# Kernel optimization log

Measured on AMD Instinct MI355X. Metric: run time of the kernel, lower is better.

Reference implementation:

```python
import jax, jax.numpy as jnp
import numpy as np

N_QUBITS = 12
N_LAYERS = 6
BATCH = 512
DIM = 2 ** N_QUBITS


def _apply_1q(psi, G, wire):
    """Apply a single-qubit gate on `wire` (wire 0 = most significant).
    psi: [B, 2^n] complex. G: [2,2] (shared) or [B,2,2] (batched)."""
    B = psi.shape[0]
    left = 2 ** wire
    psi = psi.reshape(B, left, 2, -1)
    if G.ndim == 2:
        psi = jnp.einsum('ij,bxjy->bxiy', G, psi)
    else:
        psi = jnp.einsum('bij,bxjy->bxiy', G, psi)
    return psi.reshape(B, -1)


def _apply_cnot(psi, c, t):
    """CNOT with control c, target t on [B, 2^n] state."""
    B = psi.shape[0]
    ps = psi.reshape((B,) + (2,) * N_QUBITS)
    ca, ta = c + 1, t + 1
    c0 = jnp.take(ps, 0, axis=ca)
    c1 = jnp.take(ps, 1, axis=ca)
    flip_ax = ta if ta < ca else ta - 1
    c1 = jnp.flip(c1, axis=flip_ax)  # X on target within control=1 block
    ps = jnp.stack([c0, c1], axis=ca)
    return ps.reshape(B, -1)


def _circuit(x, weights):
    B = x.shape[0]
    psi = jnp.zeros((B, DIM), jnp.complex64).at[:, 0].set(1.0)

    # AngleEmbedding: RY(x_w) on each wire (batched gate matrices)
    h = 0.5 * x
    c, s = jnp.cos(h).astype(jnp.complex64), jnp.sin(h).astype(jnp.complex64)
    for w in range(N_QUBITS):
        G = jnp.stack([jnp.stack([c[:, w], -s[:, w]], -1),
                       jnp.stack([s[:, w], c[:, w]], -1)], -2)  # [B,2,2]
        psi = _apply_1q(psi, G, w)

    # StronglyEntanglingLayers: Rot(phi,theta,omega) per wire, then ring of CNOTs
    for l in range(N_LAYERS):
        phi, theta, omega = weights[l, :, 0], weights[l, :, 1], weights[l, :, 2]
        ct = jnp.cos(0.5 * theta).astype(jnp.complex64)
        st = jnp.sin(0.5 * theta).astype(jnp.complex64)
        ep = jnp.exp(-0.5j * (phi + omega).astype(jnp.complex64))
        em = jnp.exp(0.5j * (phi - omega).astype(jnp.complex64))
        # Rot = RZ(omega) RY(theta) RZ(phi)
        m00 = ep * ct
        m01 = -em * st
        m10 = jnp.conj(em) * st
        m11 = jnp.conj(ep) * ct
        for w in range(N_QUBITS):
            G = jnp.array([[m00[w], m01[w]], [m10[w], m11[w]]], jnp.complex64)
            psi = _apply_1q(psi, G, w)
        r = l % (N_QUBITS - 1) + 1
        for w in range(N_QUBITS):
            psi = _apply_cnot(psi, w, (w + r) % N_QUBITS)

    # <Z_w> for every wire
    probs = psi.real ** 2 + psi.imag ** 2  # [B, 2^n]
    exps = []
    for w in range(N_QUBITS):
        p = probs.reshape(B, 2 ** w, 2, -1)
        exps.append(p[:, :, 0, :].sum((1, 2)) - p[:, :, 1, :].sum((1, 2)))
    return jnp.stack(exps, -1)  # [B, n_qubits]


def setup_inputs() -> dict:
    key = jax.random.key(0)
    k1, k2, k3, k4 = jax.random.split(key, 4)
    x = jax.random.uniform(k1, (BATCH, N_QUBITS), jnp.float32, -np.pi, np.pi)
    weights = jax.random.uniform(k2, (N_LAYERS, N_QUBITS, 3), jnp.float32, 0.0, 2.0 * np.pi)
    W = jax.random.normal(k3, (1, N_QUBITS), jnp.float32) * 0.3
    b = jax.random.normal(k4, (1,), jnp.float32) * 0.01
    return {"x": x, "weights": weights, "W": W, "b": b}


def reference(x, weights, W, b):
    z = _circuit(x, weights)              # [B, n_qubits]
    y = z @ W.T + b                       # [B, 1]
    return y.squeeze(-1)                  # [B]
```

## Files before the change

kernel.cpp:

```cpp
#include <hip/hip_runtime.h>
#include <stdint.h>

#define NQ 12
#define DIM 4096
#define NLAYERS 6
#define TPB 256

typedef float v2f __attribute__((ext_vector_type(2)));

struct Pass_t {
    uint32_t WT[8];
    uint32_t WL[16];
    uint32_t RT[8];
    uint32_t RL[16];
};
struct CK_t {
    Pass_t PG2, PG3;
    Pass_t P1[NLAYERS];
    uint32_t frow[NQ];
};

constexpr uint32_t G2f(uint32_t k){ return ((k&15u)<<8) | (k&0xF0u) | ((k>>8)&15u); }
constexpr uint32_t G3f(uint32_t k){ return ((k&15u)<<4) | ((k>>4)&15u) | (k&0xF00u); }

constexpr uint32_t ech_reduce(const uint32_t* v, int n, uint32_t x){
    bool ch = true;
    while (ch) {
        ch = false;
        for (int i = 0; i < n; i++)
            if (v[i] && (x ^ v[i]) < x) { x ^= v[i]; ch = true; }
    }
    return x;
}

constexpr Pass_t build_pass(const uint32_t* Mc) {
    Pass_t P{};
    uint32_t rows[12]{}; int nr = 0;
    {
        uint32_t e1[4]{}, e2[4]{}; int n1 = 0, n2 = 0;
        for (int step = 0; step < 4; step++) {
            bool found = false;
            for (int pc = 1; pc <= 3 && !found; pc++) {
                for (int a = 0; a < 12 && !found; a++)
                for (int b = (pc >= 2 ? a + 1 : 12); (pc >= 2 ? b < 12 : b == 12) && !found; b++)
                for (int c = (pc == 3 ? b + 1 : 12); (pc == 3 ? c < 12 : c == 12) && !found; c++) {
                    uint32_t m = (1u << a);
                    if (pc >= 2) m |= (1u << b);
                    if (pc == 3) m |= (1u << c);
                    uint32_t v1 = (m >> 4) & 15u;
                    uint32_t v2 = 0;
                    for (int j = 0; j < 4; j++)
                        v2 |= (uint32_t)(__builtin_popcount(m & Mc[4 + j]) & 1) << j;
                    uint32_t r1 = ech_reduce(e1, n1, v1);
                    uint32_t r2 = ech_reduce(e2, n2, v2);
                    if (r1 && r2) {
                        rows[nr++] = m; e1[n1++] = r1; e2[n2++] = r2; found = true;
                    }
                }
            }
            if (!found) { rows[nr] = 1u << (4 + nr); nr++; }
        }
    }
    {
        uint32_t ef[12]{}; int nf = 0;
        for (int i = 0; i < nr; i++) {
            uint32_t r = ech_reduce(ef, nf, rows[i]);
            if (r) ef[nf++] = r;
        }
        for (uint32_t m = 1; m < 4096u && nr < 12; m++) {
            uint32_t r = ech_reduce(ef, nf, m);
            if (r) { rows[nr++] = m; ef[nf++] = r; }
        }
    }
    uint32_t col[12]{}, rc[12]{};
    for (int j = 0; j < 12; j++) {
        uint32_t c = 0;
        for (int i = 0; i < 12; i++) c |= (uint32_t)((rows[i] >> j) & 1u) << i;
        col[j] = c;
    }
    for (int j = 0; j < 12; j++) {
        uint32_t a = 0, mc = Mc[j];
        for (int q = 0; q < 12; q++) if ((mc >> q) & 1u) a ^= col[q];
        rc[j] = a;
    }
    for (int j = 0; j < 8; j++) { P.WT[j] = col[4 + j]; P.RT[j] = rc[4 + j]; }
    for (int l = 0; l < 16; l++) {
        uint32_t aw = 0, ar = 0;
        for (int q = 0; q < 4; q++) if ((l >> q) & 1) { aw ^= col[q]; ar ^= rc[q]; }
        P.WL[l] = aw; P.RL[l] = ar;
    }
    return P;
}

constexpr CK_t build_ck() {
    CK_t ck{};
    uint32_t Acols[NLAYERS][NQ]{}, Aicol5[NQ]{};
    for (int l = 0; l < NLAYERS; l++) {
        int r = l % (NQ - 1) + 1;
        for (int q = 0; q < NQ; q++) {
            uint32_t v = 1u << q;
            for (int w = NQ - 1; w >= 0; w--) {
                int pc = NQ - 1 - w, pt = NQ - 1 - ((w + r) % NQ);
                v ^= ((v >> pc) & 1u) << pt;
            }
            Acols[l][q] = v;
            if (l == NLAYERS - 1) {
                uint32_t u = 1u << q;
                for (int w = 0; w < NQ; w++) {
                    int pc = NQ - 1 - w, pt = NQ - 1 - ((w + r) % NQ);
                    u ^= ((u >> pc) & 1u) << pt;
                }
                Aicol5[q] = u;
            }
        }
    }
    uint32_t McG2[12]{}, McG3[12]{}, Mc1[12]{};
    for (int j = 0; j < 12; j++) { McG2[j] = G2f(1u << j); McG3[j] = G3f(1u << j); }
    ck.PG2 = build_pass(McG2);
    ck.PG3 = build_pass(McG3);
    for (int l = 1; l < NLAYERS; l++) {
        for (int j = 0; j < 12; j++) Mc1[j] = G3f(G2f(Acols[l - 1][j]));
        ck.P1[l] = build_pass(Mc1);
    }
    uint32_t Mcol[NQ]{};
    for (int j = 0; j < NQ; j++) {
        uint32_t pj = G2f(G3f(1u << j));
        uint32_t M = 0;
        for (int m = 0; m < NQ; m++) if ((pj >> m) & 1u) M ^= Aicol5[m];
        Mcol[j] = M;
    }
    for (int p = 0; p < NQ; p++) {
        uint32_t s = 0;
        for (int j = 0; j < NQ; j++) s |= ((Mcol[j] >> p) & 1u) << j;
        ck.frow[p] = s;
    }
    return ck;
}
constexpr CK_t CK = build_ck();

template<int KIND, int L, int PAR>
__device__ __forceinline__ void do_pass(v2f (&Z)[16], v2f* xb, int tid) {
    constexpr Pass_t P = (KIND == 1) ? CK.P1[L] : (KIND == 2) ? CK.PG2 : CK.PG3;
    v2f* buf = xb + PAR * DIM;
    uint32_t comb = 0;
    #pragma unroll
    for (int j = 0; j < 8; j++) {
        uint32_t pk = P.WT[j] | (P.RT[j] << 16);
        comb ^= (uint32_t)(-(int)((tid >> j) & 1)) & pk;
    }
    uint32_t wbase = comb & 0xFFFu, rbase = comb >> 16;
    #pragma unroll
    for (int l = 0; l < 16; l++)
        buf[wbase ^ P.WL[l]] = Z[l];
    __syncthreads();
    #pragma unroll
    for (int l = 0; l < 16; l++)
        Z[l] = buf[rbase ^ P.RL[l]];
}

template<int L, int W, int Q>
__device__ __forceinline__ void reg_gate(v2f (&Z)[16], const float4* smat) {
    float4 m = smat[L * NQ + W];
    #pragma unroll
    for (int l = 0; l < 16; l++) {
        if (l & (1 << Q)) continue;
        int l2 = l | (1 << Q);
        v2f z0 = Z[l], z1 = Z[l2];
        v2f j0 = { -z0.y, z0.x };
        v2f j1 = { -z1.y, z1.x };
        Z[l]  = m.x * z0 + m.y * j0 + m.z * z1 + m.w * j1;
        Z[l2] = m.x * z1 - m.y * j1 - m.z * z0 + m.w * j0;
    }
}

template<int L>
__device__ __forceinline__ void do_layer(v2f (&Z)[16], const float4* smat,
                                         v2f* xb, int tid) {
    if constexpr (L > 0)
        do_pass<1, L, (3 * L - 1) & 1>(Z, xb, tid);
    reg_gate<L, 11, 0>(Z, smat);
    reg_gate<L, 10, 1>(Z, smat);
    reg_gate<L,  9, 2>(Z, smat);
    reg_gate<L,  8, 3>(Z, smat);
    do_pass<2, L, (3 * L) & 1>(Z, xb, tid);
    reg_gate<L, 3, 0>(Z, smat);
    reg_gate<L, 2, 1>(Z, smat);
    reg_gate<L, 1, 2>(Z, smat);
    reg_gate<L, 0, 3>(Z, smat);
    do_pass<3, L, (3 * L + 1) & 1>(Z, xb, tid);
    reg_gate<L, 7, 0>(Z, smat);
    reg_gate<L, 6, 1>(Z, smat);
    reg_gate<L, 5, 2>(Z, smat);
    reg_gate<L, 4, 3>(Z, smat);
}

__global__ __launch_bounds__(TPB) void qsim_kernel(
    const float* __restrict__ x,
    const float* __restrict__ weights,
    const float* __restrict__ Wp,
    const float* __restrict__ bptr,
    float* __restrict__ out)
{
    __shared__ v2f    xb[2 * DIM];
    __shared__ float4 smat[NLAYERS * NQ];
    __shared__ float  scs[NQ], sss[NQ];
    __shared__ float  red[4];

    const int tid = threadIdx.x;
    const int b   = blockIdx.x;

    if (tid < NQ) {
        float s_, c_;
        sincosf(0.5f * x[b * NQ + tid], &s_, &c_);
        scs[tid] = c_; sss[tid] = s_;
    }
    if (tid < NLAYERS * NQ) {
        float phi   = weights[tid * 3 + 0];
        float theta = weights[tid * 3 + 1];
        float omega = weights[tid * 3 + 2];
        float st, ct; sincosf(0.5f * theta, &st, &ct);
        float sp, cp; sincosf(0.5f * (phi + omega), &sp, &cp);
        float sm, cm; sincosf(0.5f * (phi - omega), &sm, &cm);
        smat[tid] = make_float4(cp * ct, -sp * ct, -cm * st, -sm * st);
    }
    __syncthreads();

    float base = 1.0f;
    #pragma unroll
    for (int p = 4; p < NQ; p++) {
        int w = NQ - 1 - p;
        base *= ((tid >> (p - 4)) & 1) ? sss[w] : scs[w];
    }
    v2f Z[16];
    #pragma unroll
    for (int l = 0; l < 16; l++) {
        float a = base;
        #pragma unroll
        for (int p = 0; p < 4; p++) {
            int w = NQ - 1 - p;
            a *= ((l >> p) & 1) ? sss[w] : scs[w];
        }
        Z[l].x = a; Z[l].y = 0.0f;
    }

    do_layer<0>(Z, smat, xb, tid);
    do_layer<1>(Z, smat, xb, tid);
    do_layer<2>(Z, smat, xb, tid);
    do_layer<3>(Z, smat, xb, tid);
    do_layer<4>(Z, smat, xb, tid);
    do_layer<5>(Z, smat, xb, tid);

    const float bv = bptr[0];
    float wb[NQ];
    #pragma unroll
    for (int p = 0; p < NQ; p++) {
        uint32_t row = CK.frow[p];
        int tp = __popc(tid & (int)(row >> 4)) & 1;
        float Wv = Wp[NQ - 1 - p];
        wb[p] = tp ? -Wv : Wv;
    }
    float acc = 0.0f;
    #pragma unroll
    for (int l = 0; l < 16; l++) {
        float coef = bv;
        #pragma unroll
        for (int p = 0; p < NQ; p++)
            coef += (__popc(l & (int)(CK.frow[p] & 15u)) & 1) ? -wb[p] : wb[p];
        acc += (Z[l].x * Z[l].x + Z[l].y * Z[l].y) * coef;
    }
    #pragma unroll
    for (int off = 32; off > 0; off >>= 1)
        acc += __shfl_down(acc, off, 64);
    if ((tid & 63) == 0) red[tid >> 6] = acc;
    __syncthreads();
    if (tid == 0) out[b] = red[0] + red[1] + red[2] + red[3];
}

extern "C" void kernel_launch(void* const* d_in, const int* in_sizes, int n_in,
                              void* d_out, int out_size, void* d_ws, size_t ws_size,
                              hipStream_t stream) {
    const float* x       = (const float*)d_in[0];
    const float* weights = (const float*)d_in[1];
    const float* W       = (const float*)d_in[2];
    const float* bptr    = (const float*)d_in[3];
    qsim_kernel<<<512, TPB, 0, stream>>>(x, weights, W, bptr, (float*)d_out);
}
```

Baseline: 93.10 us.

## Split state across 512 threads with 8 amplitudes each and four exchange passes

Doubles the thread count per block to 512 so each thread holds 8 amplitudes (3 local qubits) instead of 16. Each layer now does three or four shared-memory permutation passes instead of two or three, with new swap maps and rebuilt XOR address tables. The goal is more parallelism and lower register pressure per thread, paid for with extra barriers and more LDS traffic per layer.

```diff
diff --git a/kernel.cpp b/kernel.cpp
--- a/kernel.cpp
+++ b/kernel.cpp
@@ -4,24 +4,26 @@
 #define NQ 12
 #define DIM 4096
 #define NLAYERS 6
-#define TPB 256
+#define TPB 512
+#define NL 8
 
 typedef float v2f __attribute__((ext_vector_type(2)));
 
 struct Pass_t {
-    uint32_t WT[8];
-    uint32_t WL[16];
-    uint32_t RT[8];
-    uint32_t RL[16];
+    uint32_t WT[9];
+    uint32_t WL[NL];
+    uint32_t RT[9];
+    uint32_t RL[NL];
 };
 struct CK_t {
-    Pass_t PG2, PG3;
+    Pass_t PS1, PS2, PS3;
     Pass_t P1[NLAYERS];
     uint32_t frow[NQ];
 };
 
-constexpr uint32_t G2f(uint32_t k){ return ((k&15u)<<8) | (k&0xF0u) | ((k>>8)&15u); }
-constexpr uint32_t G3f(uint32_t k){ return ((k&15u)<<4) | ((k>>4)&15u) | (k&0xF00u); }
+constexpr uint32_t S1f(uint32_t k){ return ((k&7u)<<3) | ((k>>3)&7u) | (k & 0xFC0u); }
+constexpr uint32_t S2f(uint32_t k){ return ((k&7u)<<6) | (k & 0x38u) | ((k>>6)&7u) | (k & 0xE00u); }
+constexpr uint32_t S3f(uint32_t k){ return ((k&7u)<<9) | (k & 0x1F8u) | ((k>>9)&7u); }
 
 constexpr uint32_t ech_reduce(const uint32_t* v, int n, uint32_t x){
     bool ch = true;
@@ -47,10 +49,10 @@
                     uint32_t m = (1u << a);
                     if (pc >= 2) m |= (1u << b);
                     if (pc == 3) m |= (1u << c);
-                    uint32_t v1 = (m >> 4) & 15u;
+                    uint32_t v1 = (m >> 3) & 15u;
                     uint32_t v2 = 0;
                     for (int j = 0; j < 4; j++)
-                        v2 |= (uint32_t)(__builtin_popcount(m & Mc[4 + j]) & 1) << j;
+                        v2 |= (uint32_t)(__builtin_popcount(m & Mc[3 + j]) & 1) << j;
                     uint32_t r1 = ech_reduce(e1, n1, v1);
                     uint32_t r2 = ech_reduce(e2, n2, v2);
                     if (r1 && r2) {
@@ -58,7 +60,7 @@
                     }
                 }
             }
-            if (!found) { rows[nr] = 1u << (4 + nr); nr++; }
+            if (!found) { rows[nr] = 1u << (3 + nr); nr++; }
         }
     }
     {
@@ -83,10 +85,10 @@
         for (int q = 0; q < 12; q++) if ((mc >> q) & 1u) a ^= col[q];
         rc[j] = a;
     }
-    for (int j = 0; j < 8; j++) { P.WT[j] = col[4 + j]; P.RT[j] = rc[4 + j]; }
-    for (int l = 0; l < 16; l++) {
+    for (int j = 0; j < 9; j++) { P.WT[j] = col[3 + j]; P.RT[j] = rc[3 + j]; }
+    for (int l = 0; l < NL; l++) {
         uint32_t aw = 0, ar = 0;
-        for (int q = 0; q < 4; q++) if ((l >> q) & 1) { aw ^= col[q]; ar ^= rc[q]; }
+        for (int q = 0; q < 3; q++) if ((l >> q) & 1) { aw ^= col[q]; ar ^= rc[q]; }
         P.WL[l] = aw; P.RL[l] = ar;
     }
     return P;
@@ -114,17 +116,20 @@
             }
         }
     }
-    uint32_t McG2[12]{}, McG3[12]{}, Mc1[12]{};
-    for (int j = 0; j < 12; j++) { McG2[j] = G2f(1u << j); McG3[j] = G3f(1u << j); }
-    ck.PG2 = build_pass(McG2);
-    ck.PG3 = build_pass(McG3);
+    uint32_t Mc[12]{};
+    for (int j = 0; j < 12; j++) Mc[j] = S1f(1u << j);
+    ck.PS1 = build_pass(Mc);
+    for (int j = 0; j < 12; j++) Mc[j] = S2f(1u << j);
+    ck.PS2 = build_pass(Mc);
+    for (int j = 0; j < 12; j++) Mc[j] = S3f(1u << j);
+    ck.PS3 = build_pass(Mc);
     for (int l = 1; l < NLAYERS; l++) {
-        for (int j = 0; j < 12; j++) Mc1[j] = G3f(G2f(Acols[l - 1][j]));
-        ck.P1[l] = build_pass(Mc1);
+        for (int j = 0; j < 12; j++) Mc[j] = S3f(S2f(S1f(Acols[l - 1][j])));
+        ck.P1[l] = build_pass(Mc);
     }
     uint32_t Mcol[NQ]{};
     for (int j = 0; j < NQ; j++) {
-        uint32_t pj = G2f(G3f(1u << j));
+        uint32_t pj = S1f(S2f(S3f(1u << j)));
         uint32_t M = 0;
         for (int m = 0; m < NQ; m++) if ((pj >> m) & 1u) M ^= Aicol5[m];
         Mcol[j] = M;
@@ -139,30 +144,32 @@
 constexpr CK_t CK = build_ck();
 
 template<int KIND, int L, int PAR>
-__device__ __forceinline__ void do_pass(v2f (&Z)[16], v2f* xb, int tid) {
-    constexpr Pass_t P = (KIND == 1) ? CK.P1[L] : (KIND == 2) ? CK.PG2 : CK.PG3;
+__device__ __forceinline__ void do_pass(v2f (&Z)[NL], v2f* xb, int tid) {
+    constexpr Pass_t P = (KIND == 1) ? CK.P1[L]
+                       : (KIND == 2) ? CK.PS1
+                       : (KIND == 3) ? CK.PS2 : CK.PS3;
     v2f* buf = xb + PAR * DIM;
     uint32_t comb = 0;
     #pragma unroll
-    for (int j = 0; j < 8; j++) {
+    for (int j = 0; j < 9; j++) {
         uint32_t pk = P.WT[j] | (P.RT[j] << 16);
         comb ^= (uint32_t)(-(int)((tid >> j) & 1)) & pk;
     }
     uint32_t wbase = comb & 0xFFFu, rbase = comb >> 16;
     #pragma unroll
-    for (int l = 0; l < 16; l++)
+    for (int l = 0; l < NL; l++)
         buf[wbase ^ P.WL[l]] = Z[l];
     __syncthreads();
     #pragma unroll
-    for (int l = 0; l < 16; l++)
+    for (int l = 0; l < NL; l++)
         Z[l] = buf[rbase ^ P.RL[l]];
 }
 
 template<int L, int W, int Q>
-__device__ __forceinline__ void reg_gate(v2f (&Z)[16], const float4* smat) {
+__device__ __forceinline__ void reg_gate(v2f (&Z)[NL], const float4* smat) {
     float4 m = smat[L * NQ + W];
     #pragma unroll
-    for (int l = 0; l < 16; l++) {
+    for (int l = 0; l < NL; l++) {
         if (l & (1 << Q)) continue;
         int l2 = l | (1 << Q);
         v2f z0 = Z[l], z1 = Z[l2];
@@ -174,24 +181,25 @@
 }
 
 template<int L>
-__device__ __forceinline__ void do_layer(v2f (&Z)[16], const float4* smat,
+__device__ __forceinline__ void do_layer(v2f (&Z)[NL], const float4* smat,
                                          v2f* xb, int tid) {
     if constexpr (L > 0)
-        do_pass<1, L, (3 * L - 1) & 1>(Z, xb, tid);
+        do_pass<1, L, 1>(Z, xb, tid);
     reg_gate<L, 11, 0>(Z, smat);
     reg_gate<L, 10, 1>(Z, smat);
     reg_gate<L,  9, 2>(Z, smat);
-    reg_gate<L,  8, 3>(Z, smat);
-    do_pass<2, L, (3 * L) & 1>(Z, xb, tid);
-    reg_gate<L, 3, 0>(Z, smat);
-    reg_gate<L, 2, 1>(Z, smat);
-    reg_gate<L, 1, 2>(Z, smat);
-    reg_gate<L, 0, 3>(Z, smat);
-    do_pass<3, L, (3 * L + 1) & 1>(Z, xb, tid);
-    reg_gate<L, 7, 0>(Z, smat);
-    reg_gate<L, 6, 1>(Z, smat);
-    reg_gate<L, 5, 2>(Z, smat);
-    reg_gate<L, 4, 3>(Z, smat);
+    do_pass<2, L, 0>(Z, xb, tid);
+    reg_gate<L, 8, 0>(Z, smat);
+    reg_gate<L, 7, 1>(Z, smat);
+    reg_gate<L, 6, 2>(Z, smat);
+    do_pass<3, L, 1>(Z, xb, tid);
+    reg_gate<L, 5, 0>(Z, smat);
+    reg_gate<L, 4, 1>(Z, smat);
+    reg_gate<L, 3, 2>(Z, smat);
+    do_pass<4, L, 0>(Z, xb, tid);
+    reg_gate<L, 2, 0>(Z, smat);
+    reg_gate<L, 1, 1>(Z, smat);
+    reg_gate<L, 0, 2>(Z, smat);
 }
 
 __global__ __launch_bounds__(TPB) void qsim_kernel(
@@ -204,7 +212,7 @@
     __shared__ v2f    xb[2 * DIM];
     __shared__ float4 smat[NLAYERS * NQ];
     __shared__ float  scs[NQ], sss[NQ];
-    __shared__ float  red[4];
+    __shared__ float  red[8];
 
     const int tid = threadIdx.x;
     const int b   = blockIdx.x;
@@ -227,16 +235,16 @@
 
     float base = 1.0f;
     #pragma unroll
-    for (int p = 4; p < NQ; p++) {
-        int w = NQ - 1 - p;
-        base *= ((tid >> (p - 4)) & 1) ? sss[w] : scs[w];
-    }
-    v2f Z[16];
-    #pragma unroll
-    for (int l = 0; l < 16; l++) {
+    for (int j = 0; j < 9; j++) {
+        int w = 8 - j;
+        base *= ((tid >> j) & 1) ? sss[w] : scs[w];
+    }
+    v2f Z[NL];
+    #pragma unroll
+    for (int l = 0; l < NL; l++) {
         float a = base;
         #pragma unroll
-        for (int p = 0; p < 4; p++) {
+        for (int p = 0; p < 3; p++) {
             int w = NQ - 1 - p;
             a *= ((l >> p) & 1) ? sss[w] : scs[w];
         }
@@ -255,17 +263,17 @@
     #pragma unroll
     for (int p = 0; p < NQ; p++) {
         uint32_t row = CK.frow[p];
-        int tp = __popc(tid & (int)(row >> 4)) & 1;
+        int tp = __popc(tid & (int)(row >> 3)) & 1;
         float Wv = Wp[NQ - 1 - p];
         wb[p] = tp ? -Wv : Wv;
     }
     float acc = 0.0f;
     #pragma unroll
-    for (int l = 0; l < 16; l++) {
+    for (int l = 0; l < NL; l++) {
         float coef = bv;
         #pragma unroll
         for (int p = 0; p < NQ; p++)
-            coef += (__popc(l & (int)(CK.frow[p] & 15u)) & 1) ? -wb[p] : wb[p];
+            coef += (__popc(l & (int)(CK.frow[p] & 7u)) & 1) ? -wb[p] : wb[p];
         acc += (Z[l].x * Z[l].x + Z[l].y * Z[l].y) * coef;
     }
     #pragma unroll
@@ -273,7 +281,12 @@
         acc += __shfl_down(acc, off, 64);
     if ((tid & 63) == 0) red[tid >> 6] = acc;
     __syncthreads();
-    if (tid == 0) out[b] = red[0] + red[1] + red[2] + red[3];
+    if (tid == 0) {
+        float s = 0.0f;
+        #pragma unroll
+        for (int wv = 0; wv < TPB / 64; wv++) s += red[wv];
+        out[b] = s;
+    }
 }
 
 extern "C" void kernel_launch(void* const* d_in, const int* in_sizes, int n_in,
```

After: 93.03 us. About the same (-0.1%).
